# Kernel optimization log

Hardware: AMD Instinct MI355X
Metric: run time of the kernel (lower is better)

## Reference

```python
import jax, jax.numpy as jnp
import numpy as np

N_NODES = 50000
IN_DIM = 128
HID = 128
N_EDGES = 600000
BN_EPS = 1e-5


def setup_inputs() -> dict:
    key = jax.random.key(0)
    ks = jax.random.split(key, 8)
    x = jax.random.normal(ks[0], (N_NODES, IN_DIM), dtype=jnp.float32)
    edge_index = jax.random.randint(ks[1], (2, N_EDGES), 0, N_NODES, dtype=jnp.int64)
    s1 = 1.0 / np.sqrt(IN_DIM)
    s2 = 1.0 / np.sqrt(HID)
    W1 = jax.random.uniform(ks[2], (HID, IN_DIM), jnp.float32, -s1, s1)
    b1 = jax.random.uniform(ks[3], (HID,), jnp.float32, -s1, s1)
    gamma = jnp.ones((HID,), jnp.float32)
    beta = jnp.zeros((HID,), jnp.float32)
    W2 = jax.random.uniform(ks[4], (HID, HID), jnp.float32, -s2, s2)
    b2 = jax.random.uniform(ks[5], (HID,), jnp.float32, -s2, s2)
    Wres = jax.random.uniform(ks[6], (HID, IN_DIM), jnp.float32, -s1, s1)
    return {"x": x, "edge_index": edge_index, "W1": W1, "b1": b1,
            "gamma": gamma, "beta": beta, "W2": W2, "b2": b2, "Wres": Wres}


def reference(x, edge_index, W1, b1, gamma, beta, W2, b2, Wres):
    # GINConv aggregation (eps=0): h_v = x_v + sum_{u in N(v)} x_u
    src, dst = edge_index[0], edge_index[1]
    agg = jax.ops.segment_sum(x[src], dst, num_segments=N_NODES)  # [N, in_dim]
    h = x + agg
    # MLP: Linear -> BatchNorm (batch stats, training mode) -> LeakyReLU(0.01) -> Linear
    h = h @ W1.T + b1  # [N, hid]
    mu = jnp.mean(h, axis=0)
    var = jnp.mean(jnp.square(h - mu), axis=0)  # biased var, as torch BN training
    h = (h - mu) * jax.lax.rsqrt(var + BN_EPS) * gamma + beta
    h = jax.nn.leaky_relu(h, negative_slope=0.01)
    h = h @ W2.T + b2
    # residual projection + final leaky relu
    x_res = x @ Wres.T
    return jax.nn.leaky_relu(h + x_res, negative_slope=0.2)
```

## Files before the change

### kernel.cpp

```cpp
#include <hip/hip_runtime.h>

#define N_NODES 50000
#define N_EDGES 600000
#define BN_EPS 1e-5f
#define NBKT 782
#define BKT_CAP 1024
#define CHUNK 4096
#define CS_BLOCKS 147

typedef __bf16 bf16x8 __attribute__((ext_vector_type(8)));
typedef float f32x4 __attribute__((ext_vector_type(4)));

__device__ __forceinline__ float leaky(float v, float slope) {
    return v > 0.f ? v : v * slope;
}

__device__ __forceinline__ bf16x8 pack8(float4 v0, float4 v1) {
    bf16x8 b;
    b[0] = (__bf16)v0.x; b[1] = (__bf16)v0.y; b[2] = (__bf16)v0.z; b[3] = (__bf16)v0.w;
    b[4] = (__bf16)v1.x; b[5] = (__bf16)v1.y; b[6] = (__bf16)v1.z; b[7] = (__bf16)v1.w;
    return b;
}

__global__ __launch_bounds__(256) void k_fused(
        const int* __restrict__ ei, int* __restrict__ cnt, unsigned* __restrict__ coarse,
        const float4* __restrict__ x4, uint4* __restrict__ xb4,
        const float* __restrict__ W1, const float* __restrict__ W2,
        const float* __restrict__ Wres, uint4* __restrict__ w1f, uint4* __restrict__ w2f) {
    int tid = threadIdx.x;
    if (blockIdx.x == CS_BLOCKS + 3125) {
        #pragma unroll
        for (int i = 0; i < 8; ++i) {
            int fid = tid + i * 256;
            int lane = fid & 63, ks = (fid >> 6) & 3, jt = fid >> 8;
            const float* wp = W1 + (jt * 16 + (lane & 15)) * 128 + ks * 32 + ((lane >> 4) << 3);
            w1f[fid] = __builtin_bit_cast(uint4, pack8(*(const float4*)wp, *(const float4*)(wp + 4)));
        }
        #pragma unroll
        for (int i = 0; i < 16; ++i) {
            int fid = tid + i * 256;
            int lane = fid & 63, ks = (fid >> 6) & 7, jt = fid >> 9;
            const float* wp = (ks < 4 ? W2 : Wres) + (jt * 16 + (lane & 15)) * 128
                              + (ks & 3) * 32 + ((lane >> 4) << 3);
            w2f[fid] = __builtin_bit_cast(uint4, pack8(*(const float4*)wp, *(const float4*)(wp + 4)));
        }
        return;
    }
    if (blockIdx.x >= CS_BLOCKS) {
        int g = (blockIdx.x - CS_BLOCKS) * 256 + tid;
        float4 v0 = x4[g * 2], v1 = x4[g * 2 + 1];
        xb4[g] = __builtin_bit_cast(uint4, pack8(v0, v1));
        return;
    }
    __shared__ unsigned lcnt[NBKT];
    __shared__ unsigned lbase[NBKT];
    for (int i = tid; i < NBKT; i += 256) lcnt[i] = 0;
    __syncthreads();
    int e0 = blockIdx.x * CHUNK;
    unsigned pk[16], meta[16];
    #pragma unroll
    for (int i = 0; i < 16; ++i) {
        int e = e0 + tid + i * 256;
        if (e < N_EDGES) {
            int s = ei[e];
            int d = ei[N_EDGES + e];
            int b = d >> 6;
            pk[i] = (unsigned)s | ((unsigned)(d & 63) << 16);
            unsigned r = atomicAdd(&lcnt[b], 1u);
            meta[i] = (unsigned)b | (r << 16);
        }
    }
    __syncthreads();
    for (int b = tid; b < NBKT; b += 256) {
        unsigned c = lcnt[b];
        lbase[b] = c ? (unsigned)atomicAdd(&cnt[b], (int)c) : 0u;
    }
    __syncthreads();
    #pragma unroll
    for (int i = 0; i < 16; ++i) {
        int e = e0 + tid + i * 256;
        if (e < N_EDGES) {
            unsigned b = meta[i] & 0xFFFFu;
            unsigned p = lbase[b] + (meta[i] >> 16);
            if (p < BKT_CAP) coarse[b * BKT_CAP + p] = pk[i];
        }
    }
}

__global__ __launch_bounds__(512) void k_agg1(
        const int* __restrict__ cnt, const unsigned* __restrict__ coarse,
        const uint4* __restrict__ xb4, const uint4* __restrict__ w1f,
        const float* __restrict__ b1, __bf16* __restrict__ h1b,
        float* __restrict__ stats) {
    __shared__ unsigned hist[64];
    __shared__ unsigned offs[64];
    __shared__ unsigned short ssrc[BKT_CAP];
    __shared__ uint4 hls[1024];
    __shared__ float sred[8][64];
    __shared__ float s2red[8][64];
    int tid = threadIdx.x;
    int b = blockIdx.x;
    int m = cnt[b];
    if (m > BKT_CAP) m = BKT_CAP;

    if (tid < 64) hist[tid] = 0;
    __syncthreads();
    unsigned pk[2], rk[2];
    #pragma unroll
    for (int i = 0; i < 2; ++i) {
        int idx = tid + i * 512;
        if (idx < m) {
            pk[i] = coarse[b * BKT_CAP + idx];
            rk[i] = atomicAdd(&hist[pk[i] >> 16], 1u);
        }
    }
    __syncthreads();
    if (tid < 64) {
        unsigned v = hist[tid];
        unsigned inc = v;
        #pragma unroll
        for (int d = 1; d < 64; d <<= 1) {
            unsigned t = __shfl_up(inc, d);
            if (tid >= d) inc += t;
        }
        offs[tid] = inc - v;
    }
    __syncthreads();
    #pragma unroll
    for (int i = 0; i < 2; ++i) {
        int idx = tid + i * 512;
        if (idx < m) ssrc[offs[pk[i] >> 16] + rk[i]] = (unsigned short)(pk[i] & 0xFFFFu);
    }
    __syncthreads();

    {
        int li = tid & 15, grp = tid >> 4;
        #pragma unroll
        for (int it = 0; it < 2; ++it) {
            int dl = grp + it * 32;
            int v = b * 64 + dl;
            if (v < N_NODES) {
                bf16x8 self = __builtin_bit_cast(bf16x8, xb4[v * 16 + li]);
                float acc[8];
                #pragma unroll
                for (int k = 0; k < 8; ++k) acc[k] = (float)self[k];
                unsigned e0 = offs[dl], e1 = e0 + hist[dl];
                unsigned e = e0;
                for (; e + 4 <= e1; e += 4) {
                    int s0 = ssrc[e], s1 = ssrc[e + 1], s2 = ssrc[e + 2], s3 = ssrc[e + 3];
                    bf16x8 u0 = __builtin_bit_cast(bf16x8, xb4[s0 * 16 + li]);
                    bf16x8 u1 = __builtin_bit_cast(bf16x8, xb4[s1 * 16 + li]);
                    bf16x8 u2 = __builtin_bit_cast(bf16x8, xb4[s2 * 16 + li]);
                    bf16x8 u3 = __builtin_bit_cast(bf16x8, xb4[s3 * 16 + li]);
                    #pragma unroll
                    for (int k = 0; k < 8; ++k)
                        acc[k] += ((float)u0[k] + (float)u1[k]) + ((float)u2[k] + (float)u3[k]);
                }
                for (; e < e1; ++e) {
                    int s = ssrc[e];
                    bf16x8 u = __builtin_bit_cast(bf16x8, xb4[s * 16 + li]);
                    #pragma unroll
                    for (int k = 0; k < 8; ++k) acc[k] += (float)u[k];
                }
                bf16x8 o;
                #pragma unroll
                for (int k = 0; k < 8; ++k) o[k] = (__bf16)acc[k];
                hls[dl * 16 + (li ^ (dl & 7))] = __builtin_bit_cast(uint4, o);
            }
        }
    }
    __syncthreads();

    int wv = tid >> 6, lane = tid & 63;
    int rgrp = wv & 3, jh = wv >> 2;
    int node0 = b * 64 + rgrp * 16;
    bool valid = node0 < N_NODES;
    int dl0 = rgrp * 16 + (lane & 15);
    int q = lane >> 4;

    bf16x8 a[4];
    #pragma unroll
    for (int ks = 0; ks < 4; ++ks)
        a[ks] = __builtin_bit_cast(bf16x8, hls[dl0 * 16 + ((ks * 4 + q) ^ (dl0 & 7))]);

    #pragma unroll
    for (int jt4 = 0; jt4 < 4; ++jt4) {
        int jt = jh * 4 + jt4;
        f32x4 acc = {0.f, 0.f, 0.f, 0.f};
        #pragma unroll
        for (int ks = 0; ks < 4; ++ks) {
            bf16x8 bb = __builtin_bit_cast(bf16x8, w1f[(jt * 4 + ks) * 64 + lane]);
            acc = __builtin_amdgcn_mfma_f32_16x16x32_bf16(a[ks], bb, acc, 0, 0, 0);
        }
        int j = jt * 16 + (lane & 15);
        float bias = b1[j];
        int nb = node0 + (q << 2);
        float s = 0.f, s2 = 0.f;
        if (valid) {
            #pragma unroll
            for (int r = 0; r < 4; ++r) {
                float v = acc[r] + bias;
                h1b[(nb + r) * 128 + j] = (__bf16)v;
                s += v; s2 += v * v;
            }
        }
        s  += __shfl_down(s, 32);  s  += __shfl_down(s, 16);
        s2 += __shfl_down(s2, 32); s2 += __shfl_down(s2, 16);
        if (lane < 16) {
            sred[wv][jt4 * 16 + (lane & 15)] = s;
            s2red[wv][jt4 * 16 + (lane & 15)] = s2;
        }
    }
    __syncthreads();
    if (tid < 128) {
        int half = tid >> 6, jj = tid & 63, w0 = half * 4;
        atomicAdd(&stats[tid],
                  sred[w0][jj] + sred[w0 + 1][jj] + sred[w0 + 2][jj] + sred[w0 + 3][jj]);
        atomicAdd(&stats[128 + tid],
                  s2red[w0][jj] + s2red[w0 + 1][jj] + s2red[w0 + 2][jj] + s2red[w0 + 3][jj]);
    }
}

__global__ __launch_bounds__(256) void k_gemm2(
        const uint4* __restrict__ h1b4, const uint4* __restrict__ xb4,
        const uint4* __restrict__ w2f, const float* __restrict__ b2,
        const float* __restrict__ stats, const float* __restrict__ gamma,
        const float* __restrict__ beta, float* __restrict__ out) {
    __shared__ float bl[128], scl[128], shl[128];
    int tid = threadIdx.x;
    if (tid < 128) {
        float inv = 1.f / (float)N_NODES;
        float mu = stats[tid] * inv;
        float var = stats[128 + tid] * inv - mu * mu;
        float rs = rsqrtf(var + BN_EPS);
        float sc = gamma[tid] * rs;
        bl[tid]  = b2[tid];
        scl[tid] = sc;
        shl[tid] = beta[tid] - mu * sc;
    }
    __syncthreads();

    int wv = tid >> 6, lane = tid & 63;
    int strip = blockIdx.x * 4 + wv;
    if (strip >= 3125) return;
    int node0 = strip * 16;
    int rbase = (node0 + (lane & 15)) * 16 + (lane >> 4);
    int kbase = (lane >> 4) << 3;

    bf16x8 a[8];
    #pragma unroll
    for (int ks = 0; ks < 4; ++ks) {
        bf16x8 hv = __builtin_bit_cast(bf16x8, h1b4[rbase + ks * 4]);
        #pragma unroll
        for (int e = 0; e < 8; ++e) {
            int k = kbase + ks * 32 + e;
            float t = (float)hv[e] * scl[k] + shl[k];
            a[ks][e] = (__bf16)leaky(t, 0.01f);
        }
    }
    #pragma unroll
    for (int ks = 0; ks < 4; ++ks)
        a[4 + ks] = __builtin_bit_cast(bf16x8, xb4[rbase + ks * 4]);

    #pragma unroll
    for (int jt = 0; jt < 8; ++jt) {
        f32x4 acc = {0.f, 0.f, 0.f, 0.f};
        #pragma unroll
        for (int ks = 0; ks < 8; ++ks) {
            bf16x8 b = __builtin_bit_cast(bf16x8, w2f[(jt * 8 + ks) * 64 + lane]);
            acc = __builtin_amdgcn_mfma_f32_16x16x32_bf16(a[ks], b, acc, 0, 0, 0);
        }
        int j = jt * 16 + (lane & 15);
        float bias = bl[j];
        int nb = node0 + ((lane >> 4) << 2);
        #pragma unroll
        for (int r = 0; r < 4; ++r) {
            float v = acc[r] + bias;
            out[(nb + r) * 128 + j] = leaky(v, 0.2f);
        }
    }
}

extern "C" void kernel_launch(void* const* d_in, const int* in_sizes, int n_in,
                              void* d_out, int out_size, void* d_ws, size_t ws_size,
                              hipStream_t stream) {
    const float* x     = (const float*)d_in[0];
    const int*   ei    = (const int*)d_in[1];
    const float* W1    = (const float*)d_in[2];
    const float* b1    = (const float*)d_in[3];
    const float* gamma = (const float*)d_in[4];
    const float* beta  = (const float*)d_in[5];
    const float* W2    = (const float*)d_in[6];
    const float* b2    = (const float*)d_in[7];
    const float* Wres  = (const float*)d_in[8];
    float* out = (float*)d_out;

    char* ws = (char*)d_ws;
    uint4*    xb4    = (uint4*)ws;
    __bf16*   h1b    = (__bf16*)(ws + 25600000);
    unsigned* coarse = (unsigned*)(ws + 38400000);
    int*      cnt    = (int*)(ws + 41700000);
    float*    stats  = (float*)(ws + 41700000 + NBKT * 4);
    uint4*    w1f    = (uint4*)(ws + 42000000);
    uint4*    w2f    = w1f + 2048;

    hipMemsetAsync(cnt, 0, (NBKT + 512) * 4, stream);
    k_fused<<<CS_BLOCKS + 3125 + 1, 256, 0, stream>>>(ei, cnt, coarse, (const float4*)x, xb4,
                                                      W1, W2, Wres, w1f, w2f);
    k_agg1<<<NBKT, 512, 0, stream>>>(cnt, coarse, xb4, w1f, b1, h1b, stats);
    k_gemm2<<<782, 256, 0, stream>>>((const uint4*)h1b, xb4, w2f, b2, stats, gamma, beta, out);
}
```

Measured before the change: 97.84 us.

## Merge all stages into one cooperative persistent kernel with grid syncs

```diff
diff --git a/kernel.cpp b/kernel.cpp
--- a/kernel.cpp
+++ b/kernel.cpp
@@ -1,12 +1,19 @@
 #include <hip/hip_runtime.h>
+#include <hip/hip_cooperative_groups.h>
 
 #define N_NODES 50000
 #define N_EDGES 600000
 #define BN_EPS 1e-5f
-#define NBKT 782
-#define BKT_CAP 1024
+#define NBKT 1563
+#define BKT_CAP 512
 #define CHUNK 4096
-#define CS_BLOCKS 147
+#define CS_UNITS 147
+#define CVT_UNITS 1563
+#define RPK_UNITS 12
+#define V0 (CVT_UNITS + RPK_UNITS + 1)
+#define V3 391
+
+namespace cg = cooperative_groups;
 
 typedef __bf16 bf16x8 __attribute__((ext_vector_type(8)));
 typedef float f32x4 __attribute__((ext_vector_type(4)));
@@ -22,132 +29,133 @@
     return b;
 }
 
-__global__ __launch_bounds__(256) void k_fused(
-        const int* __restrict__ ei, int* __restrict__ cnt, unsigned* __restrict__ coarse,
-        const float4* __restrict__ x4, uint4* __restrict__ xb4,
+union SMem {
+    struct { unsigned lcnt[NBKT]; unsigned lbase[NBKT]; } sp;
+    struct { unsigned hist[32]; unsigned offs[32]; unsigned short ssrc[BKT_CAP];
+             uint4 hls[512]; float sred[8][32]; float s2red[8][32]; } ag;
+    struct { float bl[128], scl[128], shl[128]; } g2;
+};
+
+__global__ __launch_bounds__(512, 4) void k_all(
+        const int* __restrict__ ei, const float4* __restrict__ x4,
         const float* __restrict__ W1, const float* __restrict__ W2,
-        const float* __restrict__ Wres, uint4* __restrict__ w1f, uint4* __restrict__ w2f) {
+        const float* __restrict__ Wres, const float* __restrict__ b1,
+        const float* __restrict__ b2, const float* __restrict__ gamma,
+        const float* __restrict__ beta, float* __restrict__ out,
+        char* __restrict__ ws) {
+    __shared__ SMem sm;
+    uint4*    xb4    = (uint4*)ws;
+    __bf16*   h1b    = (__bf16*)(ws + 25600000);
+    unsigned* coarse = (unsigned*)(ws + 38400000);
+    int*      cnt    = (int*)(ws + 41700000);
+    float*    stats  = (float*)(ws + 41706400);
+    uint4*    w1f    = (uint4*)(ws + 41800000);
+    uint4*    w2f    = w1f + 2048;
+
+    cg::grid_group grid = cg::this_grid();
     int tid = threadIdx.x;
-    if (blockIdx.x == CS_BLOCKS + 3125) {
+    int G = gridDim.x;
+
+    for (int vb = blockIdx.x; vb < V0; vb += G) {
+        if (vb < CVT_UNITS) {
+            int g = vb * 512 + tid;
+            if (g < 800000) {
+                float4 v0 = x4[g * 2], v1 = x4[g * 2 + 1];
+                xb4[g] = __builtin_bit_cast(uint4, pack8(v0, v1));
+            }
+        } else if (vb < CVT_UNITS + RPK_UNITS) {
+            int fid = (vb - CVT_UNITS) * 512 + tid;
+            if (fid < 2048) {
+                int lane = fid & 63, ks = (fid >> 6) & 3, jt = fid >> 8;
+                const float* wp = W1 + (jt * 16 + (lane & 15)) * 128 + ks * 32 + ((lane >> 4) << 3);
+                w1f[fid] = __builtin_bit_cast(uint4, pack8(*(const float4*)wp, *(const float4*)(wp + 4)));
+            } else {
+                int f2 = fid - 2048;
+                int lane = f2 & 63, ks = (f2 >> 6) & 7, jt = f2 >> 9;
+                const float* wp = (ks < 4 ? W2 : Wres) + (jt * 16 + (lane & 15)) * 128
+                                  + (ks & 3) * 32 + ((lane >> 4) << 3);
+                w2f[f2] = __builtin_bit_cast(uint4, pack8(*(const float4*)wp, *(const float4*)(wp + 4)));
+            }
+        } else {
+            for (int i = tid; i < 2112; i += 512) cnt[i] = 0;
+        }
+    }
+    grid.sync();
+
+    for (int vb = blockIdx.x; vb < CS_UNITS; vb += G) {
+        for (int i = tid; i < NBKT; i += 512) sm.sp.lcnt[i] = 0;
+        __syncthreads();
+        int e0 = vb * CHUNK;
+        unsigned pk[8], meta[8];
         #pragma unroll
         for (int i = 0; i < 8; ++i) {
-            int fid = tid + i * 256;
-            int lane = fid & 63, ks = (fid >> 6) & 3, jt = fid >> 8;
-            const float* wp = W1 + (jt * 16 + (lane & 15)) * 128 + ks * 32 + ((lane >> 4) << 3);
-            w1f[fid] = __builtin_bit_cast(uint4, pack8(*(const float4*)wp, *(const float4*)(wp + 4)));
-        }
-        #pragma unroll
-        for (int i = 0; i < 16; ++i) {
-            int fid = tid + i * 256;
-            int lane = fid & 63, ks = (fid >> 6) & 7, jt = fid >> 9;
-            const float* wp = (ks < 4 ? W2 : Wres) + (jt * 16 + (lane & 15)) * 128
-                              + (ks & 3) * 32 + ((lane >> 4) << 3);
-            w2f[fid] = __builtin_bit_cast(uint4, pack8(*(const float4*)wp, *(const float4*)(wp + 4)));
-        }
-        return;
-    }
-    if (blockIdx.x >= CS_BLOCKS) {
-        int g = (blockIdx.x - CS_BLOCKS) * 256 + tid;
-        float4 v0 = x4[g * 2], v1 = x4[g * 2 + 1];
-        xb4[g] = __builtin_bit_cast(uint4, pack8(v0, v1));
-        return;
-    }
-    __shared__ unsigned lcnt[NBKT];
-    __shared__ unsigned lbase[NBKT];
-    for (int i = tid; i < NBKT; i += 256) lcnt[i] = 0;
-    __syncthreads();
-    int e0 = blockIdx.x * CHUNK;
-    unsigned pk[16], meta[16];
-    #pragma unroll
-    for (int i = 0; i < 16; ++i) {
-        int e = e0 + tid + i * 256;
-        if (e < N_EDGES) {
-            int s = ei[e];
-            int d = ei[N_EDGES + e];
-            int b = d >> 6;
-            pk[i] = (unsigned)s | ((unsigned)(d & 63) << 16);
-            unsigned r = atomicAdd(&lcnt[b], 1u);
-            meta[i] = (unsigned)b | (r << 16);
-        }
-    }
-    __syncthreads();
-    for (int b = tid; b < NBKT; b += 256) {
-        unsigned c = lcnt[b];
-        lbase[b] = c ? (unsigned)atomicAdd(&cnt[b], (int)c) : 0u;
-    }
-    __syncthreads();
-    #pragma unroll
-    for (int i = 0; i < 16; ++i) {
-        int e = e0 + tid + i * 256;
-        if (e < N_EDGES) {
-            unsigned b = meta[i] & 0xFFFFu;
-            unsigned p = lbase[b] + (meta[i] >> 16);
-            if (p < BKT_CAP) coarse[b * BKT_CAP + p] = pk[i];
-        }
-    }
-}
-
-__global__ __launch_bounds__(512) void k_agg1(
-        const int* __restrict__ cnt, const unsigned* __restrict__ coarse,
-        const uint4* __restrict__ xb4, const uint4* __restrict__ w1f,
-        const float* __restrict__ b1, __bf16* __restrict__ h1b,
-        float* __restrict__ stats) {
-    __shared__ unsigned hist[64];
-    __shared__ unsigned offs[64];
-    __shared__ unsigned short ssrc[BKT_CAP];
-    __shared__ uint4 hls[1024];
-    __shared__ float sred[8][64];
-    __shared__ float s2red[8][64];
-    int tid = threadIdx.x;
-    int b = blockIdx.x;
-    int m = cnt[b];
-    if (m > BKT_CAP) m = BKT_CAP;
-
-    if (tid < 64) hist[tid] = 0;
-    __syncthreads();
-    unsigned pk[2], rk[2];
-    #pragma unroll
-    for (int i = 0; i < 2; ++i) {
-        int idx = tid + i * 512;
-        if (idx < m) {
-            pk[i] = coarse[b * BKT_CAP + idx];
-            rk[i] = atomicAdd(&hist[pk[i] >> 16], 1u);
-        }
-    }
-    __syncthreads();
-    if (tid < 64) {
-        unsigned v = hist[tid];
-        unsigned inc = v;
-        #pragma unroll
-        for (int d = 1; d < 64; d <<= 1) {
-            unsigned t = __shfl_up(inc, d);
-            if (tid >= d) inc += t;
-        }
-        offs[tid] = inc - v;
-    }
-    __syncthreads();
-    #pragma unroll
-    for (int i = 0; i < 2; ++i) {
-        int idx = tid + i * 512;
-        if (idx < m) ssrc[offs[pk[i] >> 16] + rk[i]] = (unsigned short)(pk[i] & 0xFFFFu);
-    }
-    __syncthreads();
-
-    {
-        int li = tid & 15, grp = tid >> 4;
-        #pragma unroll
-        for (int it = 0; it < 2; ++it) {
-            int dl = grp + it * 32;
-            int v = b * 64 + dl;
+            int e = e0 + tid + i * 512;
+            if (e < N_EDGES) {
+                int s = ei[e];
+                int d = ei[N_EDGES + e];
+                int b = d >> 5;
+                pk[i] = (unsigned)s | ((unsigned)(d & 31) << 16);
+                unsigned r = atomicAdd(&sm.sp.lcnt[b], 1u);
+                meta[i] = (unsigned)b | (r << 16);
+            }
+        }
+        __syncthreads();
+        for (int b = tid; b < NBKT; b += 512) {
+            unsigned c = sm.sp.lcnt[b];
+            sm.sp.lbase[b] = c ? (unsigned)atomicAdd(&cnt[b], (int)c) : 0u;
+        }
+        __syncthreads();
+        #pragma unroll
+        for (int i = 0; i < 8; ++i) {
+            int e = e0 + tid + i * 512;
+            if (e < N_EDGES) {
+                unsigned b = meta[i] & 0xFFFFu;
+                unsigned p = sm.sp.lbase[b] + (meta[i] >> 16);
+                if (p < BKT_CAP) coarse[b * BKT_CAP + p] = pk[i];
+            }
+        }
+        __syncthreads();
+    }
+    grid.sync();
+
+    for (int b = blockIdx.x; b < NBKT; b += G) {
+        int m = cnt[b];
+        if (m > BKT_CAP) m = BKT_CAP;
+        if (tid < 32) sm.ag.hist[tid] = 0;
+        __syncthreads();
+        unsigned pk = 0, rk = 0;
+        if (tid < m) {
+            pk = coarse[b * BKT_CAP + tid];
+            rk = atomicAdd(&sm.ag.hist[pk >> 16], 1u);
+        }
+        __syncthreads();
+        if (tid < 32) {
+            unsigned v = sm.ag.hist[tid];
+            unsigned inc = v;
+            #pragma unroll
+            for (int d = 1; d < 32; d <<= 1) {
+                unsigned t = __shfl_up(inc, d);
+                if (tid >= d) inc += t;
+            }
+            sm.ag.offs[tid] = inc - v;
+        }
+        __syncthreads();
+        if (tid < m) sm.ag.ssrc[sm.ag.offs[pk >> 16] + rk] = (unsigned short)(pk & 0xFFFFu);
+        __syncthreads();
+
+        {
+            int li = tid & 15, dl = tid >> 4;
+            int v = b * 32 + dl;
             if (v < N_NODES) {
                 bf16x8 self = __builtin_bit_cast(bf16x8, xb4[v * 16 + li]);
                 float acc[8];
                 #pragma unroll
                 for (int k = 0; k < 8; ++k) acc[k] = (float)self[k];
-                unsigned e0 = offs[dl], e1 = e0 + hist[dl];
+                unsigned e0 = sm.ag.offs[dl], e1 = e0 + sm.ag.hist[dl];
                 unsigned e = e0;
                 for (; e + 4 <= e1; e += 4) {
-                    int s0 = ssrc[e], s1 = ssrc[e + 1], s2 = ssrc[e + 2], s3 = ssrc[e + 3];
+                    int s0 = sm.ag.ssrc[e],     s1 = sm.ag.ssrc[e + 1];
+                    int s2 = sm.ag.ssrc[e + 2], s3 = sm.ag.ssrc[e + 3];
                     bf16x8 u0 = __builtin_bit_cast(bf16x8, xb4[s0 * 16 + li]);
                     bf16x8 u1 = __builtin_bit_cast(bf16x8, xb4[s1 * 16 + li]);
                     bf16x8 u2 = __builtin_bit_cast(bf16x8, xb4[s2 * 16 + li]);
@@ -157,7 +165,7 @@
                         acc[k] += ((float)u0[k] + (float)u1[k]) + ((float)u2[k] + (float)u3[k]);
                 }
                 for (; e < e1; ++e) {
-                    int s = ssrc[e];
+                    int s = sm.ag.ssrc[e];
                     bf16x8 u = __builtin_bit_cast(bf16x8, xb4[s * 16 + li]);
                     #pragma unroll
                     for (int k = 0; k < 8; ++k) acc[k] += (float)u[k];
@@ -165,118 +173,116 @@
                 bf16x8 o;
                 #pragma unroll
                 for (int k = 0; k < 8; ++k) o[k] = (__bf16)acc[k];
-                hls[dl * 16 + (li ^ (dl & 7))] = __builtin_bit_cast(uint4, o);
-            }
-        }
-    }
-    __syncthreads();
-
-    int wv = tid >> 6, lane = tid & 63;
-    int rgrp = wv & 3, jh = wv >> 2;
-    int node0 = b * 64 + rgrp * 16;
-    bool valid = node0 < N_NODES;
-    int dl0 = rgrp * 16 + (lane & 15);
-    int q = lane >> 4;
-
-    bf16x8 a[4];
-    #pragma unroll
-    for (int ks = 0; ks < 4; ++ks)
-        a[ks] = __builtin_bit_cast(bf16x8, hls[dl0 * 16 + ((ks * 4 + q) ^ (dl0 & 7))]);
-
-    #pragma unroll
-    for (int jt4 = 0; jt4 < 4; ++jt4) {
-        int jt = jh * 4 + jt4;
-        f32x4 acc = {0.f, 0.f, 0.f, 0.f};
-        #pragma unroll
-        for (int ks = 0; ks < 4; ++ks) {
-            bf16x8 bb = __builtin_bit_cast(bf16x8, w1f[(jt * 4 + ks) * 64 + lane]);
-            acc = __builtin_amdgcn_mfma_f32_16x16x32_bf16(a[ks], bb, acc, 0, 0, 0);
-        }
-        int j = jt * 16 + (lane & 15);
-        float bias = b1[j];
-        int nb = node0 + (q << 2);
-        float s = 0.f, s2 = 0.f;
-        if (valid) {
-            #pragma unroll
-            for (int r = 0; r < 4; ++r) {
-                float v = acc[r] + bias;
-                h1b[(nb + r) * 128 + j] = (__bf16)v;
-                s += v; s2 += v * v;
-            }
-        }
-        s  += __shfl_down(s, 32);  s  += __shfl_down(s, 16);
-        s2 += __shfl_down(s2, 32); s2 += __shfl_down(s2, 16);
-        if (lane < 16) {
-            sred[wv][jt4 * 16 + (lane & 15)] = s;
-            s2red[wv][jt4 * 16 + (lane & 15)] = s2;
-        }
-    }
-    __syncthreads();
-    if (tid < 128) {
-        int half = tid >> 6, jj = tid & 63, w0 = half * 4;
-        atomicAdd(&stats[tid],
-                  sred[w0][jj] + sred[w0 + 1][jj] + sred[w0 + 2][jj] + sred[w0 + 3][jj]);
-        atomicAdd(&stats[128 + tid],
-                  s2red[w0][jj] + s2red[w0 + 1][jj] + s2red[w0 + 2][jj] + s2red[w0 + 3][jj]);
-    }
-}
-
-__global__ __launch_bounds__(256) void k_gemm2(
-        const uint4* __restrict__ h1b4, const uint4* __restrict__ xb4,
-        const uint4* __restrict__ w2f, const float* __restrict__ b2,
-        const float* __restrict__ stats, const float* __restrict__ gamma,
-        const float* __restrict__ beta, float* __restrict__ out) {
-    __shared__ float bl[128], scl[128], shl[128];
-    int tid = threadIdx.x;
+                sm.ag.hls[dl * 16 + (li ^ (dl & 7))] = __builtin_bit_cast(uint4, o);
+            }
+        }
+        __syncthreads();
+
+        {
+            int wv = tid >> 6, lane = tid & 63;
+            int rgrp = wv & 1, jq = wv >> 1;
+            int node0 = b * 32 + rgrp * 16;
+            bool valid = node0 < N_NODES;
+            int dl0 = rgrp * 16 + (lane & 15);
+            int q = lane >> 4;
+
+            bf16x8 a[4];
+            #pragma unroll
+            for (int ks = 0; ks < 4; ++ks)
+                a[ks] = __builtin_bit_cast(bf16x8, sm.ag.hls[dl0 * 16 + ((ks * 4 + q) ^ (dl0 & 7))]);
+
+            #pragma unroll
+            for (int jt2 = 0; jt2 < 2; ++jt2) {
+                int jt = jq * 2 + jt2;
+                f32x4 acc = {0.f, 0.f, 0.f, 0.f};
+                #pragma unroll
+                for (int ks = 0; ks < 4; ++ks) {
+                    bf16x8 bb = __builtin_bit_cast(bf16x8, w1f[(jt * 4 + ks) * 64 + lane]);
+                    acc = __builtin_amdgcn_mfma_f32_16x16x32_bf16(a[ks], bb, acc, 0, 0, 0);
+                }
+                int j = jt * 16 + (lane & 15);
+                float bias = b1[j];
+                int nb = node0 + (q << 2);
+                float s = 0.f, s2 = 0.f;
+                if (valid) {
+                    #pragma unroll
+                    for (int r = 0; r < 4; ++r) {
+                        float v = acc[r] + bias;
+                        h1b[(nb + r) * 128 + j] = (__bf16)v;
+                        s += v; s2 += v * v;
+                    }
+                }
+                s  += __shfl_down(s, 32);  s  += __shfl_down(s, 16);
+                s2 += __shfl_down(s2, 32); s2 += __shfl_down(s2, 16);
+                if (lane < 16) {
+                    sm.ag.sred[wv][jt2 * 16 + (lane & 15)] = s;
+                    sm.ag.s2red[wv][jt2 * 16 + (lane & 15)] = s2;
+                }
+            }
+        }
+        __syncthreads();
+        if (tid < 128) {
+            int jt = tid >> 4, jq2 = jt >> 1, jt2 = jt & 1, col = tid & 15;
+            float s  = sm.ag.sred[jq2 * 2][jt2 * 16 + col]  + sm.ag.sred[jq2 * 2 + 1][jt2 * 16 + col];
+            float s2 = sm.ag.s2red[jq2 * 2][jt2 * 16 + col] + sm.ag.s2red[jq2 * 2 + 1][jt2 * 16 + col];
+            atomicAdd(&stats[tid], s);
+            atomicAdd(&stats[128 + tid], s2);
+        }
+        __syncthreads();
+    }
+    grid.sync();
+
     if (tid < 128) {
         float inv = 1.f / (float)N_NODES;
         float mu = stats[tid] * inv;
         float var = stats[128 + tid] * inv - mu * mu;
         float rs = rsqrtf(var + BN_EPS);
         float sc = gamma[tid] * rs;
-        bl[tid]  = b2[tid];
-        scl[tid] = sc;
-        shl[tid] = beta[tid] - mu * sc;
+        sm.g2.bl[tid]  = b2[tid];
+        sm.g2.scl[tid] = sc;
+        sm.g2.shl[tid] = beta[tid] - mu * sc;
     }
     __syncthreads();
 
-    int wv = tid >> 6, lane = tid & 63;
-    int strip = blockIdx.x * 4 + wv;
-    if (strip >= 3125) return;
-    int node0 = strip * 16;
-    int rbase = (node0 + (lane & 15)) * 16 + (lane >> 4);
-    int kbase = (lane >> 4) << 3;
-
-    bf16x8 a[8];
-    #pragma unroll
-    for (int ks = 0; ks < 4; ++ks) {
-        bf16x8 hv = __builtin_bit_cast(bf16x8, h1b4[rbase + ks * 4]);
-        #pragma unroll
-        for (int e = 0; e < 8; ++e) {
-            int k = kbase + ks * 32 + e;
-            float t = (float)hv[e] * scl[k] + shl[k];
-            a[ks][e] = (__bf16)leaky(t, 0.01f);
-        }
-    }
-    #pragma unroll
-    for (int ks = 0; ks < 4; ++ks)
-        a[4 + ks] = __builtin_bit_cast(bf16x8, xb4[rbase + ks * 4]);
-
-    #pragma unroll
-    for (int jt = 0; jt < 8; ++jt) {
-        f32x4 acc = {0.f, 0.f, 0.f, 0.f};
-        #pragma unroll
-        for (int ks = 0; ks < 8; ++ks) {
-            bf16x8 b = __builtin_bit_cast(bf16x8, w2f[(jt * 8 + ks) * 64 + lane]);
-            acc = __builtin_amdgcn_mfma_f32_16x16x32_bf16(a[ks], b, acc, 0, 0, 0);
-        }
-        int j = jt * 16 + (lane & 15);
-        float bias = bl[j];
-        int nb = node0 + ((lane >> 4) << 2);
-        #pragma unroll
-        for (int r = 0; r < 4; ++r) {
-            float v = acc[r] + bias;
-            out[(nb + r) * 128 + j] = leaky(v, 0.2f);
+    for (int vb = blockIdx.x; vb < V3; vb += G) {
+        int wv = tid >> 6, lane = tid & 63;
+        int strip = vb * 8 + wv;
+        if (strip >= 3125) continue;
+        int node0 = strip * 16;
+        int rbase = (node0 + (lane & 15)) * 16 + (lane >> 4);
+        int kbase = (lane >> 4) << 3;
+
+        bf16x8 a[8];
+        #pragma unroll
+        for (int ks = 0; ks < 4; ++ks) {
+            bf16x8 hv = __builtin_bit_cast(bf16x8, ((const uint4*)h1b)[rbase + ks * 4]);
+            #pragma unroll
+            for (int e = 0; e < 8; ++e) {
+                int k = kbase + ks * 32 + e;
+                float t = (float)hv[e] * sm.g2.scl[k] + sm.g2.shl[k];
+                a[ks][e] = (__bf16)leaky(t, 0.01f);
+            }
+        }
+        #pragma unroll
+        for (int ks = 0; ks < 4; ++ks)
+            a[4 + ks] = __builtin_bit_cast(bf16x8, xb4[rbase + ks * 4]);
+
+        #pragma unroll
+        for (int jt = 0; jt < 8; ++jt) {
+            f32x4 acc = {0.f, 0.f, 0.f, 0.f};
+            #pragma unroll
+            for (int ks = 0; ks < 8; ++ks) {
+                bf16x8 bb = __builtin_bit_cast(bf16x8, w2f[(jt * 8 + ks) * 64 + lane]);
+                acc = __builtin_amdgcn_mfma_f32_16x16x32_bf16(a[ks], bb, acc, 0, 0, 0);
+            }
+            int j = jt * 16 + (lane & 15);
+            float bias = sm.g2.bl[j];
+            int nb = node0 + ((lane >> 4) << 2);
+            #pragma unroll
+            for (int r = 0; r < 4; ++r) {
+                float v = acc[r] + bias;
+                out[(nb + r) * 128 + j] = leaky(v, 0.2f);
+            }
         }
     }
 }
@@ -284,29 +290,26 @@
 extern "C" void kernel_launch(void* const* d_in, const int* in_sizes, int n_in,
                               void* d_out, int out_size, void* d_ws, size_t ws_size,
                               hipStream_t stream) {
-    const float* x     = (const float*)d_in[0];
-    const int*   ei    = (const int*)d_in[1];
-    const float* W1    = (const float*)d_in[2];
-    const float* b1    = (const float*)d_in[3];
-    const float* gamma = (const float*)d_in[4];
-    const float* beta  = (const float*)d_in[5];
-    const float* W2    = (const float*)d_in[6];
-    const float* b2    = (const float*)d_in[7];
-    const float* Wres  = (const float*)d_in[8];
+    const int*    ei    = (const int*)d_in[1];
+    const float4* x4    = (const float4*)d_in[0];
+    const float*  W1    = (const float*)d_in[2];
+    const float*  b1    = (const float*)d_in[3];
+    const float*  gamma = (const float*)d_in[4];
+    const float*  beta  = (const float*)d_in[5];
+    const float*  W2    = (const float*)d_in[6];
+    const float*  b2    = (const float*)d_in[7];
+    const float*  Wres  = (const float*)d_in[8];
     float* out = (float*)d_out;
-
-    char* ws = (char*)d_ws;
-    uint4*    xb4    = (uint4*)ws;
-    __bf16*   h1b    = (__bf16*)(ws + 25600000);
-    unsigned* coarse = (unsigned*)(ws + 38400000);
-    int*      cnt    = (int*)(ws + 41700000);
-    float*    stats  = (float*)(ws + 41700000 + NBKT * 4);
-    uint4*    w1f    = (uint4*)(ws + 42000000);
-    uint4*    w2f    = w1f + 2048;
-
-    hipMemsetAsync(cnt, 0, (NBKT + 512) * 4, stream);
-    k_fused<<<CS_BLOCKS + 3125 + 1, 256, 0, stream>>>(ei, cnt, coarse, (const float4*)x, xb4,
-                                                      W1, W2, Wres, w1f, w2f);
-    k_agg1<<<NBKT, 512, 0, stream>>>(cnt, coarse, xb4, w1f, b1, h1b, stats);
-    k_gemm2<<<782, 256, 0, stream>>>((const uint4*)h1b, xb4, w2f, b2, stats, gamma, beta, out);
+    char*  ws  = (char*)d_ws;
+
+    int nb = 0;
+    if (hipOccupancyMaxActiveBlocksPerMultiprocessor(&nb, k_all, 512, 0) != hipSuccess || nb < 1)
+        nb = 1;
+    int G = nb * 256;
+    if (G > V0) G = V0;
+
+    void* kargs[] = {(void*)&ei, (void*)&x4, (void*)&W1, (void*)&W2, (void*)&Wres,
+                     (void*)&b1, (void*)&b2, (void*)&gamma, (void*)&beta,
+                     (void*)&out, (void*)&ws};
+    hipLaunchCooperativeKernel((void*)k_all, dim3(G), dim3(512), kargs, 0, stream);
 }
```

Result: slower. 242.9 us (+148.3%).
